# Performance work log

Measured on AMD Instinct MI355X. Metric: run time of the kernel, lower is better.

## Reference

```python
import jax, jax.numpy as jnp
import numpy as np

N, F_IN, UNITS, HEADS = 4096, 128, 64, 4
EDGE_P = 0.01  # adjacency density


def setup_inputs() -> dict:
    key = jax.random.key(0)
    k1, k2, k3, k4, k5 = jax.random.split(key, 5)
    inputs = jax.random.normal(k1, (N, F_IN), dtype=jnp.float32)
    adj = jax.random.bernoulli(k2, EDGE_P, (N, N)).astype(jnp.float32)
    # glorot-normal-ish parameter scales
    w = jax.random.normal(k3, (F_IN, UNITS), dtype=jnp.float32) * np.float32(np.sqrt(2.0 / (F_IN + UNITS)))
    attn_w1 = jax.random.normal(k4, (UNITS, HEADS), dtype=jnp.float32) * np.float32(np.sqrt(2.0 / (UNITS + HEADS)))
    attn_w2 = jax.random.normal(k5, (UNITS, HEADS), dtype=jnp.float32) * np.float32(np.sqrt(2.0 / (UNITS + HEADS)))
    return {"inputs": inputs, "adj": adj, "w": w, "attn_w1": attn_w1, "attn_w2": attn_w2}


def reference(inputs, adj, w, attn_w1, attn_w2):
    # dropout=0, bias=0, final_layer=False, activation=relu
    x = inputs @ w                                  # [N, U]
    e1 = x @ attn_w1                                # [N, H]
    e2 = x @ attn_w2                                # [N, H]
    # coeffs[i, j, h] = relu(e1[i, h] + e2[j, h])
    coeffs = jax.nn.relu(e1[:, None, :] + e2[None, :, :])   # [N, N, H]
    # NOTE: original multiplies by adj (zeros -> logit 0, not -inf) then softmax over j
    scores = adj[:, :, None] * coeffs               # [N, N, H]
    attn = jax.nn.softmax(scores, axis=1)           # normalize over neighbors j
    # per-head aggregation, concat heads -> [N, H*U] (head-major blocks)
    out = jnp.einsum("ijh,ju->ihu", attn, x).reshape(N, HEADS * UNITS)
    return jax.nn.relu(out)
```

## Files before the change

kernel.cpp:

```cpp
#include <hip/hip_runtime.h>
#include <hip/hip_bf16.h>

#define N_NODES 4096
#define F_IN    128
#define UNITS   64
#define HEADS   4

__global__ __launch_bounds__(256) void k1(const float* __restrict__ inputs,
                                          const float* __restrict__ w,
                                          const float* __restrict__ aw1,
                                          const float* __restrict__ aw2,
                                          float* __restrict__ x,
                                          float* __restrict__ e1,
                                          float* __restrict__ e2,
                                          float* __restrict__ partial) {
    __shared__ float w_lds[F_IN * UNITS];
    __shared__ float in_lds[16 * F_IN];
    __shared__ float x_lds[16 * 65];
    __shared__ float aw_lds[2 * UNITS * HEADS];

    const int t = threadIdx.x;
    const int b = blockIdx.x;
    const int row0 = b * 16;

    {
        const float4* src = (const float4*)w;
        float4* dst = (float4*)w_lds;
        for (int idx = t; idx < F_IN * UNITS / 4; idx += 256) dst[idx] = src[idx];
    }
    {
        const float4* src = (const float4*)(inputs + (size_t)row0 * F_IN);
        float4* dst = (float4*)in_lds;
        for (int idx = t; idx < 16 * F_IN / 4; idx += 256) dst[idx] = src[idx];
    }
    if (t < UNITS * HEADS) {
        aw_lds[t] = aw1[t];
        aw_lds[UNITS * HEADS + t] = aw2[t];
    }
    __syncthreads();

    const int u = t & 63;
    const int rg = t >> 6;
    float acc0 = 0.f, acc1 = 0.f, acc2 = 0.f, acc3 = 0.f;
    const float4* r0 = (const float4*)(in_lds + (rg * 4 + 0) * F_IN);
    const float4* r1 = (const float4*)(in_lds + (rg * 4 + 1) * F_IN);
    const float4* r2 = (const float4*)(in_lds + (rg * 4 + 2) * F_IN);
    const float4* r3 = (const float4*)(in_lds + (rg * 4 + 3) * F_IN);
#pragma unroll 8
    for (int c = 0; c < F_IN / 4; c++) {
        const int k4 = c * 4;
        const float w0 = w_lds[(k4 + 0) * UNITS + u];
        const float w1 = w_lds[(k4 + 1) * UNITS + u];
        const float w2 = w_lds[(k4 + 2) * UNITS + u];
        const float w3 = w_lds[(k4 + 3) * UNITS + u];
        float4 a;
        a = r0[c]; acc0 = fmaf(a.w, w3, fmaf(a.z, w2, fmaf(a.y, w1, fmaf(a.x, w0, acc0))));
        a = r1[c]; acc1 = fmaf(a.w, w3, fmaf(a.z, w2, fmaf(a.y, w1, fmaf(a.x, w0, acc1))));
        a = r2[c]; acc2 = fmaf(a.w, w3, fmaf(a.z, w2, fmaf(a.y, w1, fmaf(a.x, w0, acc2))));
        a = r3[c]; acc3 = fmaf(a.w, w3, fmaf(a.z, w2, fmaf(a.y, w1, fmaf(a.x, w0, acc3))));
    }
    x_lds[(rg * 4 + 0) * 65 + u] = acc0;
    x_lds[(rg * 4 + 1) * 65 + u] = acc1;
    x_lds[(rg * 4 + 2) * 65 + u] = acc2;
    x_lds[(rg * 4 + 3) * 65 + u] = acc3;
    x[(size_t)(row0 + rg * 4 + 0) * UNITS + u] = acc0;
    x[(size_t)(row0 + rg * 4 + 1) * UNITS + u] = acc1;
    x[(size_t)(row0 + rg * 4 + 2) * UNITS + u] = acc2;
    x[(size_t)(row0 + rg * 4 + 3) * UNITS + u] = acc3;
    __syncthreads();

    if (t < 128) {
        const int r = t >> 3;
        const int rem = t & 7;
        const int h = rem & 3;
        const bool first = rem < 4;
        const float* aw = aw_lds + (first ? 0 : UNITS * HEADS);
        float s = 0.f;
#pragma unroll 8
        for (int uu = 0; uu < UNITS; uu++)
            s += x_lds[r * 65 + uu] * aw[uu * HEADS + h];
        (first ? e1 : e2)[(size_t)(row0 + r) * HEADS + h] = s;
    }

    if (t < 64) {
        float s = 0.f;
#pragma unroll
        for (int r = 0; r < 16; r++) s += x_lds[r * 65 + t];
        partial[b * 64 + t] = s;
    }
}

__global__ __launch_bounds__(256) void k1b(const float* __restrict__ partial,
                                           float* __restrict__ S) {
    __shared__ float red[4][64];
    const int u = threadIdx.x & 63;
    const int q = threadIdx.x >> 6;
    float s = 0.f;
#pragma unroll 8
    for (int b = q; b < 256; b += 4) s += partial[b * 64 + u];
    red[q][u] = s;
    __syncthreads();
    if (threadIdx.x < 64) S[u] = red[0][u] + red[1][u] + red[2][u] + red[3][u];
}

__global__ __launch_bounds__(256) void k2(const float* __restrict__ adj,
                                          const float* __restrict__ x,
                                          const float* __restrict__ e1,
                                          const float* __restrict__ e2,
                                          const float* __restrict__ S,
                                          float* __restrict__ out) {
    __shared__ unsigned short nbr[N_NODES];
    __shared__ float2 pairs[HEADS][64];
    __shared__ int cnt;

    const int i = blockIdx.x;
    const int t = threadIdx.x;
    const int lane = t & 63;
    const int h = t >> 6;

    if (t == 0) cnt = 0;
    __syncthreads();

    const float4* arow = (const float4*)(adj + (size_t)i * N_NODES);
    const float4 v0 = arow[t];
    const float4 v1 = arow[t + 256];
    const float4 v2 = arow[t + 512];
    const float4 v3 = arow[t + 768];

    const unsigned long long b0  = __ballot(v0.x != 0.f);
    const unsigned long long b1  = __ballot(v0.y != 0.f);
    const unsigned long long b2  = __ballot(v0.z != 0.f);
    const unsigned long long b3  = __ballot(v0.w != 0.f);
    const unsigned long long b4  = __ballot(v1.x != 0.f);
    const unsigned long long b5  = __ballot(v1.y != 0.f);
    const unsigned long long b6  = __ballot(v1.z != 0.f);
    const unsigned long long b7  = __ballot(v1.w != 0.f);
    const unsigned long long b8  = __ballot(v2.x != 0.f);
    const unsigned long long b9  = __ballot(v2.y != 0.f);
    const unsigned long long b10 = __ballot(v2.z != 0.f);
    const unsigned long long b11 = __ballot(v2.w != 0.f);
    const unsigned long long b12 = __ballot(v3.x != 0.f);
    const unsigned long long b13 = __ballot(v3.y != 0.f);
    const unsigned long long b14 = __ballot(v3.z != 0.f);
    const unsigned long long b15 = __ballot(v3.w != 0.f);

    const int tot = __popcll(b0) + __popcll(b1) + __popcll(b2) + __popcll(b3)
                  + __popcll(b4) + __popcll(b5) + __popcll(b6) + __popcll(b7)
                  + __popcll(b8) + __popcll(b9) + __popcll(b10) + __popcll(b11)
                  + __popcll(b12) + __popcll(b13) + __popcll(b14) + __popcll(b15);

    int wbase = 0;
    if (lane == 0) wbase = atomicAdd(&cnt, tot);
    wbase = __shfl(wbase, 0);

    const unsigned long long lt = (1ull << lane) - 1ull;
    {
        int off = wbase;
        const int g0 = t * 4, g1 = (t + 256) * 4, g2 = (t + 512) * 4, g3 = (t + 768) * 4;
        if (v0.x != 0.f) nbr[off + __popcll(b0  & lt)] = (unsigned short)(g0 + 0); off += __popcll(b0);
        if (v0.y != 0.f) nbr[off + __popcll(b1  & lt)] = (unsigned short)(g0 + 1); off += __popcll(b1);
        if (v0.z != 0.f) nbr[off + __popcll(b2  & lt)] = (unsigned short)(g0 + 2); off += __popcll(b2);
        if (v0.w != 0.f) nbr[off + __popcll(b3  & lt)] = (unsigned short)(g0 + 3); off += __popcll(b3);
        if (v1.x != 0.f) nbr[off + __popcll(b4  & lt)] = (unsigned short)(g1 + 0); off += __popcll(b4);
        if (v1.y != 0.f) nbr[off + __popcll(b5  & lt)] = (unsigned short)(g1 + 1); off += __popcll(b5);
        if (v1.z != 0.f) nbr[off + __popcll(b6  & lt)] = (unsigned short)(g1 + 2); off += __popcll(b6);
        if (v1.w != 0.f) nbr[off + __popcll(b7  & lt)] = (unsigned short)(g1 + 3); off += __popcll(b7);
        if (v2.x != 0.f) nbr[off + __popcll(b8  & lt)] = (unsigned short)(g2 + 0); off += __popcll(b8);
        if (v2.y != 0.f) nbr[off + __popcll(b9  & lt)] = (unsigned short)(g2 + 1); off += __popcll(b9);
        if (v2.z != 0.f) nbr[off + __popcll(b10 & lt)] = (unsigned short)(g2 + 2); off += __popcll(b10);
        if (v2.w != 0.f) nbr[off + __popcll(b11 & lt)] = (unsigned short)(g2 + 3); off += __popcll(b11);
        if (v3.x != 0.f) nbr[off + __popcll(b12 & lt)] = (unsigned short)(g3 + 0); off += __popcll(b12);
        if (v3.y != 0.f) nbr[off + __popcll(b13 & lt)] = (unsigned short)(g3 + 1); off += __popcll(b13);
        if (v3.z != 0.f) nbr[off + __popcll(b14 & lt)] = (unsigned short)(g3 + 2); off += __popcll(b14);
        if (v3.w != 0.f) nbr[off + __popcll(b15 & lt)] = (unsigned short)(g3 + 3); off += __popcll(b15);
    }
    __syncthreads();

    const int n = cnt;
    const float e1h = e1[(size_t)i * HEADS + h];

    float acc = 0.f;
    float den_lane = 0.f;

    for (int base = 0; base < n; base += 64) {
        const int m = min(n - base, 64);
        int j = 0;
        float wv = 0.f;
        if (lane < m) {
            j = nbr[base + lane];
            const float e2h = e2[(size_t)j * HEADS + h];
            wv = __expf(fmaxf(e1h + e2h, 0.f)) - 1.f;
            den_lane += wv;
        }
        pairs[h][lane] = make_float2(__int_as_float(j), wv);

#pragma unroll 4
        for (int k = 0; k < m; k++) {
            const float2 p = pairs[h][k];
            const int jk = __float_as_int(p.x);
            acc = fmaf(p.y, x[(jk << 6) + lane], acc);
        }
    }

    float den = den_lane;
    den += __shfl_xor(den, 32);
    den += __shfl_xor(den, 16);
    den += __shfl_xor(den, 8);
    den += __shfl_xor(den, 4);
    den += __shfl_xor(den, 2);
    den += __shfl_xor(den, 1);

    const float numer = S[lane] + acc;
    const float denom = (float)N_NODES + den;
    out[(size_t)i * (HEADS * UNITS) + t] = fmaxf(numer / denom, 0.f);
}

extern "C" void kernel_launch(void* const* d_in, const int* in_sizes, int n_in,
                              void* d_out, int out_size, void* d_ws, size_t ws_size,
                              hipStream_t stream) {
    const float* inputs = (const float*)d_in[0];
    const float* adj    = (const float*)d_in[1];
    const float* w      = (const float*)d_in[2];
    const float* aw1    = (const float*)d_in[3];
    const float* aw2    = (const float*)d_in[4];
    float* out = (float*)d_out;

    float* ws = (float*)d_ws;
    float* x       = ws;
    float* e1      = ws + 262144;
    float* e2      = ws + 262144 + 16384;
    float* partial = ws + 262144 + 2 * 16384;
    float* S       = ws + 262144 + 3 * 16384;

    k1<<<256, 256, 0, stream>>>(inputs, w, aw1, aw2, x, e1, e2, partial);
    k1b<<<1, 256, 0, stream>>>(partial, S);
    k2<<<N_NODES, 256, 0, stream>>>(adj, x, e1, e2, S, out);
}
```

Measured before the change: 119.9 us.

## Share gathered x rows across heads in k2 and halve k1 row tile

In k2, each wave previously handled one head and gathered x[j] separately, so every neighbor row was loaded four times. Now all four head weights are computed once per neighbor into LDS as a float4. Each wave takes a strided subset of neighbors and keeps accumulators for all heads, and partial sums are combined across waves through LDS. k1 now uses 8 rows per block over 512 blocks to get more parallelism, which doubles the partial buffer and the k1b reduction and adds block barriers per chunk in k2.

```diff
diff --git a/kernel.cpp b/kernel.cpp
--- a/kernel.cpp
+++ b/kernel.cpp
@@ -5,6 +5,7 @@
 #define F_IN    128
 #define UNITS   64
 #define HEADS   4
+#define K2_CHUNK 256
 
 __global__ __launch_bounds__(256) void k1(const float* __restrict__ inputs,
                                           const float* __restrict__ w,
@@ -15,13 +16,13 @@
                                           float* __restrict__ e2,
                                           float* __restrict__ partial) {
     __shared__ float w_lds[F_IN * UNITS];
-    __shared__ float in_lds[16 * F_IN];
-    __shared__ float x_lds[16 * 65];
+    __shared__ float in_lds[8 * F_IN];
+    __shared__ float x_lds[8 * 65];
     __shared__ float aw_lds[2 * UNITS * HEADS];
 
     const int t = threadIdx.x;
     const int b = blockIdx.x;
-    const int row0 = b * 16;
+    const int row0 = b * 8;
 
     {
         const float4* src = (const float4*)w;
@@ -31,7 +32,7 @@
     {
         const float4* src = (const float4*)(inputs + (size_t)row0 * F_IN);
         float4* dst = (float4*)in_lds;
-        for (int idx = t; idx < 16 * F_IN / 4; idx += 256) dst[idx] = src[idx];
+        dst[t] = src[t];
     }
     if (t < UNITS * HEADS) {
         aw_lds[t] = aw1[t];
@@ -41,11 +42,9 @@
 
     const int u = t & 63;
     const int rg = t >> 6;
-    float acc0 = 0.f, acc1 = 0.f, acc2 = 0.f, acc3 = 0.f;
-    const float4* r0 = (const float4*)(in_lds + (rg * 4 + 0) * F_IN);
-    const float4* r1 = (const float4*)(in_lds + (rg * 4 + 1) * F_IN);
-    const float4* r2 = (const float4*)(in_lds + (rg * 4 + 2) * F_IN);
-    const float4* r3 = (const float4*)(in_lds + (rg * 4 + 3) * F_IN);
+    float acc0 = 0.f, acc1 = 0.f;
+    const float4* r0 = (const float4*)(in_lds + (rg * 2 + 0) * F_IN);
+    const float4* r1 = (const float4*)(in_lds + (rg * 2 + 1) * F_IN);
 #pragma unroll 8
     for (int c = 0; c < F_IN / 4; c++) {
         const int k4 = c * 4;
@@ -56,20 +55,14 @@
         float4 a;
         a = r0[c]; acc0 = fmaf(a.w, w3, fmaf(a.z, w2, fmaf(a.y, w1, fmaf(a.x, w0, acc0))));
         a = r1[c]; acc1 = fmaf(a.w, w3, fmaf(a.z, w2, fmaf(a.y, w1, fmaf(a.x, w0, acc1))));
-        a = r2[c]; acc2 = fmaf(a.w, w3, fmaf(a.z, w2, fmaf(a.y, w1, fmaf(a.x, w0, acc2))));
-        a = r3[c]; acc3 = fmaf(a.w, w3, fmaf(a.z, w2, fmaf(a.y, w1, fmaf(a.x, w0, acc3))));
-    }
-    x_lds[(rg * 4 + 0) * 65 + u] = acc0;
-    x_lds[(rg * 4 + 1) * 65 + u] = acc1;
-    x_lds[(rg * 4 + 2) * 65 + u] = acc2;
-    x_lds[(rg * 4 + 3) * 65 + u] = acc3;
-    x[(size_t)(row0 + rg * 4 + 0) * UNITS + u] = acc0;
-    x[(size_t)(row0 + rg * 4 + 1) * UNITS + u] = acc1;
-    x[(size_t)(row0 + rg * 4 + 2) * UNITS + u] = acc2;
-    x[(size_t)(row0 + rg * 4 + 3) * UNITS + u] = acc3;
-    __syncthreads();
-
-    if (t < 128) {
+    }
+    x_lds[(rg * 2 + 0) * 65 + u] = acc0;
+    x_lds[(rg * 2 + 1) * 65 + u] = acc1;
+    x[(size_t)(row0 + rg * 2 + 0) * UNITS + u] = acc0;
+    x[(size_t)(row0 + rg * 2 + 1) * UNITS + u] = acc1;
+    __syncthreads();
+
+    if (t < 64) {
         const int r = t >> 3;
         const int rem = t & 7;
         const int h = rem & 3;
@@ -85,7 +78,7 @@
     if (t < 64) {
         float s = 0.f;
 #pragma unroll
-        for (int r = 0; r < 16; r++) s += x_lds[r * 65 + t];
+        for (int r = 0; r < 8; r++) s += x_lds[r * 65 + t];
         partial[b * 64 + t] = s;
     }
 }
@@ -97,7 +90,7 @@
     const int q = threadIdx.x >> 6;
     float s = 0.f;
 #pragma unroll 8
-    for (int b = q; b < 256; b += 4) s += partial[b * 64 + u];
+    for (int b = q; b < 512; b += 4) s += partial[b * 64 + u];
     red[q][u] = s;
     __syncthreads();
     if (threadIdx.x < 64) S[u] = red[0][u] + red[1][u] + red[2][u] + red[3][u];
@@ -110,13 +103,15 @@
                                           const float* __restrict__ S,
                                           float* __restrict__ out) {
     __shared__ unsigned short nbr[N_NODES];
-    __shared__ float2 pairs[HEADS][64];
+    __shared__ float4 wgt[K2_CHUNK];
+    __shared__ float red[4][HEADS * UNITS];
+    __shared__ float4 denred[4];
     __shared__ int cnt;
 
     const int i = blockIdx.x;
     const int t = threadIdx.x;
     const int lane = t & 63;
-    const int h = t >> 6;
+    const int wid = t >> 6;
 
     if (t == 0) cnt = 0;
     __syncthreads();
@@ -177,40 +172,71 @@
     __syncthreads();
 
     const int n = cnt;
-    const float e1h = e1[(size_t)i * HEADS + h];
-
-    float acc = 0.f;
-    float den_lane = 0.f;
-
-    for (int base = 0; base < n; base += 64) {
-        const int m = min(n - base, 64);
-        int j = 0;
-        float wv = 0.f;
-        if (lane < m) {
-            j = nbr[base + lane];
-            const float e2h = e2[(size_t)j * HEADS + h];
-            wv = __expf(fmaxf(e1h + e2h, 0.f)) - 1.f;
-            den_lane += wv;
+    const float4 e1v = *(const float4*)(e1 + (size_t)i * HEADS);
+
+    float a0 = 0.f, a1 = 0.f, a2 = 0.f, a3 = 0.f;
+    float4 dpart = make_float4(0.f, 0.f, 0.f, 0.f);
+
+    for (int base = 0; base < n; base += K2_CHUNK) {
+        const int m = min(n - base, K2_CHUNK);
+
+        for (int k = t; k < m; k += 256) {
+            const int j = nbr[base + k];
+            const float4 e2v = *(const float4*)(e2 + (size_t)j * HEADS);
+            float4 wv;
+            wv.x = __expf(fmaxf(e1v.x + e2v.x, 0.f)) - 1.f;
+            wv.y = __expf(fmaxf(e1v.y + e2v.y, 0.f)) - 1.f;
+            wv.z = __expf(fmaxf(e1v.z + e2v.z, 0.f)) - 1.f;
+            wv.w = __expf(fmaxf(e1v.w + e2v.w, 0.f)) - 1.f;
+            wgt[k] = wv;
+            dpart.x += wv.x; dpart.y += wv.y; dpart.z += wv.z; dpart.w += wv.w;
         }
-        pairs[h][lane] = make_float2(__int_as_float(j), wv);
+        __syncthreads();
 
 #pragma unroll 4
-        for (int k = 0; k < m; k++) {
-            const float2 p = pairs[h][k];
-            const int jk = __float_as_int(p.x);
-            acc = fmaf(p.y, x[(jk << 6) + lane], acc);
+        for (int k = wid; k < m; k += 4) {
+            const float4 p = wgt[k];
+            const int j = nbr[base + k];
+            const float xv = x[(j << 6) + lane];
+            a0 = fmaf(p.x, xv, a0);
+            a1 = fmaf(p.y, xv, a1);
+            a2 = fmaf(p.z, xv, a2);
+            a3 = fmaf(p.w, xv, a3);
         }
-    }
-
-    float den = den_lane;
-    den += __shfl_xor(den, 32);
-    den += __shfl_xor(den, 16);
-    den += __shfl_xor(den, 8);
-    den += __shfl_xor(den, 4);
-    den += __shfl_xor(den, 2);
-    den += __shfl_xor(den, 1);
-
-    const float numer = S[lane] + acc;
+        __syncthreads();
+    }
+
+    dpart.x += __shfl_xor(dpart.x, 32); dpart.y += __shfl_xor(dpart.y, 32);
+    dpart.z += __shfl_xor(dpart.z, 32); dpart.w += __shfl_xor(dpart.w, 32);
+    dpart.x += __shfl_xor(dpart.x, 16); dpart.y += __shfl_xor(dpart.y, 16);
+    dpart.z += __shfl_xor(dpart.z, 16); dpart.w += __shfl_xor(dpart.w, 16);
+    dpart.x += __shfl_xor(dpart.x, 8);  dpart.y += __shfl_xor(dpart.y, 8);
+    dpart.z += __shfl_xor(dpart.z, 8);  dpart.w += __shfl_xor(dpart.w, 8);
+    dpart.x += __shfl_xor(dpart.x, 4);  dpart.y += __shfl_xor(dpart.y, 4);
+    dpart.z += __shfl_xor(dpart.z, 4);  dpart.w += __shfl_xor(dpart.w, 4);
+    dpart.x += __shfl_xor(dpart.x, 2);  dpart.y += __shfl_xor(dpart.y, 2);
+    dpart.z += __shfl_xor(dpart.z, 2);  dpart.w += __shfl_xor(dpart.w, 2);
+    dpart.x += __shfl_xor(dpart.x, 1);  dpart.y += __shfl_xor(dpart.y, 1);
+    dpart.z += __shfl_xor(dpart.z, 1);  dpart.w += __shfl_xor(dpart.w, 1);
+
+    red[wid][0 * 64 + lane] = a0;
+    red[wid][1 * 64 + lane] = a1;
+    red[wid][2 * 64 + lane] = a2;
+    red[wid][3 * 64 + lane] = a3;
+    if (lane == 0) denred[wid] = dpart;
+    __syncthreads();
+
+    const int h = wid;
+    const int u = lane;
+    const float accsum = red[0][h * 64 + u] + red[1][h * 64 + u]
+                       + red[2][h * 64 + u] + red[3][h * 64 + u];
+    const float* d0 = (const float*)&denred[0];
+    const float* d1 = (const float*)&denred[1];
+    const float* d2 = (const float*)&denred[2];
+    const float* d3 = (const float*)&denred[3];
+    const float den = d0[h] + d1[h] + d2[h] + d3[h];
+
+    const float numer = S[u] + accsum;
     const float denom = (float)N_NODES + den;
     out[(size_t)i * (HEADS * UNITS) + t] = fmaxf(numer / denom, 0.f);
 }
@@ -230,9 +256,9 @@
     float* e1      = ws + 262144;
     float* e2      = ws + 262144 + 16384;
     float* partial = ws + 262144 + 2 * 16384;
-    float* S       = ws + 262144 + 3 * 16384;
-
-    k1<<<256, 256, 0, stream>>>(inputs, w, aw1, aw2, x, e1, e2, partial);
+    float* S       = ws + 262144 + 2 * 16384 + 32768;
+
+    k1<<<512, 256, 0, stream>>>(inputs, w, aw1, aw2, x, e1, e2, partial);
     k1b<<<1, 256, 0, stream>>>(partial, S);
     k2<<<N_NODES, 256, 0, stream>>>(adj, x, e1, e2, S, out);
 }
```

New measurement: 118.2 us, median of 2. Within noise of the previous version (-1.4%).
